# Kernel optimization log

Measured on AMD Instinct MI355X. Metric: run time of the kernel, lower is better.

## Reference

```python
import jax, jax.numpy as jnp
import numpy as np

B, T, U, D, INNER, VOCAB = 4, 256, 64, 512, 512, 2048

def setup_inputs() -> dict:
    key = jax.random.key(0)
    ks = jax.random.split(key, 6)
    return {
        "enc_state": jax.random.normal(ks[0], (B, T, D), jnp.float32),
        "dec_state": jax.random.normal(ks[1], (B, U, D), jnp.float32),
        "W1": jax.random.normal(ks[2], (2 * D, INNER), jnp.float32) * 0.02,
        "b1": jax.random.normal(ks[3], (INNER,), jnp.float32) * 0.02,
        "W2": jax.random.normal(ks[4], (INNER, VOCAB), jnp.float32) * 0.02,
        "b2": jax.random.normal(ks[5], (VOCAB,), jnp.float32) * 0.02,
    }

def reference(enc_state, dec_state, W1, b1, W2, b2):
    # concat([enc, dec]) @ W1 == enc @ W1[:D] + dec @ W1[D:]  (same math,
    # avoids materializing the [B,T,U,2D] repeat+cat tensor)
    d = enc_state.shape[-1]
    We, Wd = W1[:d], W1[d:]
    enc_proj = jnp.einsum('btd,dk->btk', enc_state, We)           # [B,T,INNER]
    dec_proj = jnp.einsum('bud,dk->buk', dec_state, Wd)           # [B,U,INNER]
    hidden = jnp.tanh(enc_proj[:, :, None, :] + dec_proj[:, None, :, :] + b1)  # [B,T,U,INNER]
    logits = jnp.einsum('btuk,kv->btuv', hidden, W2) + b2          # [B,T,U,VOCAB]
    return logits
```

## Files before the change

kernel.cpp:

```cpp
#include <hip/hip_runtime.h>
#include <hip/hip_bf16.h>

#define B_  4
#define T_  256
#define U_  64
#define D_  512
#define INNER_ 512
#define VOCAB_ 2048

typedef __attribute__((ext_vector_type(8))) short short8;
typedef __attribute__((ext_vector_type(4))) float f32x4;

__global__ __launch_bounds__(256) void proj_kernel(
    const float* __restrict__ enc, const float* __restrict__ dec,
    const float* __restrict__ W1, const float* __restrict__ b1,
    float* __restrict__ encP, float* __restrict__ decPb) {
  int ct = blockIdx.x;
  int rt = blockIdx.y;
  const float* src; float* dst; int kOff; int addB1; int rowBase;
  if (rt < 64) { src = enc; dst = encP; kOff = 0; addB1 = 0; rowBase = rt * 16; }
  else { src = dec; dst = decPb; kOff = D_; addB1 = 1; rowBase = (rt - 64) * 16; }

  __shared__ float As[16][D_];
  int tid = threadIdx.x;
  const float4* s4 = (const float4*)(src + (size_t)rowBase * D_);
  float4* a4 = (float4*)(&As[0][0]);
#pragma unroll
  for (int i = 0; i < 8; i++) a4[tid + 256 * i] = s4[tid + 256 * i];
  __syncthreads();

  int colQ = (tid & 31) * 4;
  int col = ct * 128 + colQ;
  int r0 = (tid >> 5) * 2;
  float a00=0,a01=0,a02=0,a03=0, a10=0,a11=0,a12=0,a13=0;
  const float* Wp = W1 + (size_t)kOff * INNER_ + col;
#pragma unroll 4
  for (int k = 0; k < D_; k++) {
    float4 w = *(const float4*)(Wp + (size_t)k * INNER_);
    float e0 = As[r0][k], e1 = As[r0 + 1][k];
    a00 += e0 * w.x; a01 += e0 * w.y; a02 += e0 * w.z; a03 += e0 * w.w;
    a10 += e1 * w.x; a11 += e1 * w.y; a12 += e1 * w.z; a13 += e1 * w.w;
  }
  float4 bb = {0,0,0,0};
  if (addB1) bb = *(const float4*)(b1 + col);
  float4 o0 = {a00 + bb.x, a01 + bb.y, a02 + bb.z, a03 + bb.w};
  float4 o1 = {a10 + bb.x, a11 + bb.y, a12 + bb.z, a13 + bb.w};
  *(float4*)(dst + (size_t)(rowBase + r0) * INNER_ + col) = o0;
  *(float4*)(dst + (size_t)(rowBase + r0 + 1) * INNER_ + col) = o1;
}

__global__ __launch_bounds__(256) void w2t_kernel(
    const float* __restrict__ W2, __hip_bfloat16* __restrict__ W2T) {
  __shared__ float tile[32][33];
  int vBase = blockIdx.x * 32;
  int kBase = blockIdx.y * 32;
  int tx = threadIdx.x & 31, ty = threadIdx.x >> 5;
#pragma unroll
  for (int i = 0; i < 32; i += 8)
    tile[ty + i][tx] = W2[(size_t)(kBase + ty + i) * VOCAB_ + vBase + tx];
  __syncthreads();
#pragma unroll
  for (int i = 0; i < 32; i += 8)
    W2T[(size_t)(vBase + ty + i) * INNER_ + kBase + tx] = __float2bfloat16(tile[tx][ty + i]);
}

__global__ __launch_bounds__(256) void hidden_kernel(
    const float* __restrict__ encP, const float* __restrict__ decPb,
    __hip_bfloat16* __restrict__ H) {
  int gid = blockIdx.x * 256 + threadIdx.x;
  int k0 = (gid & 63) * 8;
  int r = gid >> 6;
  int u = r & 63;
  int bt = r >> 6;
  int b = bt >> 8;
  const float4* e = (const float4*)(encP + (size_t)bt * 512 + k0);
  const float4* dv = (const float4*)(decPb + (size_t)(b * 64 + u) * 512 + k0);
  float4 e0 = e[0], e1 = e[1];
  float4 d0 = dv[0], d1 = dv[1];
  union { __hip_bfloat16 h[8]; uint4 v; } p;
  p.h[0] = __float2bfloat16(tanhf(e0.x + d0.x));
  p.h[1] = __float2bfloat16(tanhf(e0.y + d0.y));
  p.h[2] = __float2bfloat16(tanhf(e0.z + d0.z));
  p.h[3] = __float2bfloat16(tanhf(e0.w + d0.w));
  p.h[4] = __float2bfloat16(tanhf(e1.x + d1.x));
  p.h[5] = __float2bfloat16(tanhf(e1.y + d1.y));
  p.h[6] = __float2bfloat16(tanhf(e1.z + d1.z));
  p.h[7] = __float2bfloat16(tanhf(e1.w + d1.w));
  *(uint4*)((__hip_bfloat16*)H + (size_t)r * 512 + k0) = p.v;
}

__device__ inline void gload_lds16(const void* g, void* l) {
  __builtin_amdgcn_global_load_lds(
      (const __attribute__((address_space(1))) unsigned int*)g,
      (__attribute__((address_space(3))) unsigned int*)l, 16, 0, 0);
}

__global__ __launch_bounds__(256) void joint_gemm(
    const __hip_bfloat16* __restrict__ H, const __hip_bfloat16* __restrict__ W2T,
    const float* __restrict__ b2, float* __restrict__ out) {
  __shared__ __hip_bfloat16 As[128 * 64];
  __shared__ __hip_bfloat16 Bs[128 * 64];
  int ct = blockIdx.x;
  int rt = blockIdx.y;
  int tid = threadIdx.x;
  int wave = tid >> 6, lane = tid & 63;
  int wm = wave & 1, wn = wave >> 1;
  int rowBase = rt * 128, colBase = ct * 128;

  f32x4 acc[4][4];
#pragma unroll
  for (int ni = 0; ni < 4; ni++) {
    float bval = b2[colBase + wn * 64 + ni * 16 + (lane & 15)];
#pragma unroll
    for (int mi = 0; mi < 4; mi++) acc[mi][ni] = (f32x4){bval, bval, bval, bval};
  }

  int lrow = lane >> 3;
  int lk = (lane & 7) * 8;
  const __hip_bfloat16* Ag = H + (size_t)rowBase * 512;
  const __hip_bfloat16* Bg = W2T + (size_t)colBase * 512;

  for (int kt = 0; kt < 8; kt++) {
    int kOff = kt * 64;
    __syncthreads();
#pragma unroll
    for (int rnd = 0; rnd < 4; rnd++) {
      int rbase = wave * 8 + rnd * 32;
      gload_lds16(Ag + (size_t)(rbase + lrow) * 512 + kOff + lk, &As[rbase * 64]);
      gload_lds16(Bg + (size_t)(rbase + lrow) * 512 + kOff + lk, &Bs[rbase * 64]);
    }
    __syncthreads();
#pragma unroll
    for (int ks = 0; ks < 2; ks++) {
      short8 a[4], b[4];
      int kk = ks * 32 + (lane >> 4) * 8;
#pragma unroll
      for (int mi = 0; mi < 4; mi++)
        a[mi] = *(const short8*)&As[(wm * 64 + mi * 16 + (lane & 15)) * 64 + kk];
#pragma unroll
      for (int ni = 0; ni < 4; ni++)
        b[ni] = *(const short8*)&Bs[(wn * 64 + ni * 16 + (lane & 15)) * 64 + kk];
#pragma unroll
      for (int mi = 0; mi < 4; mi++)
#pragma unroll
        for (int ni = 0; ni < 4; ni++)
          acc[mi][ni] = __builtin_amdgcn_mfma_f32_16x16x32_bf16(a[mi], b[ni], acc[mi][ni], 0, 0, 0);
    }
  }

#pragma unroll
  for (int mi = 0; mi < 4; mi++) {
    int row = rowBase + wm * 64 + mi * 16 + ((lane >> 4) << 2);
#pragma unroll
    for (int ni = 0; ni < 4; ni++) {
      int col = colBase + wn * 64 + ni * 16 + (lane & 15);
#pragma unroll
      for (int j = 0; j < 4; j++)
        out[(size_t)(row + j) * VOCAB_ + col] = acc[mi][ni][j];
    }
  }
}

extern "C" void kernel_launch(void* const* d_in, const int* in_sizes, int n_in,
                              void* d_out, int out_size, void* d_ws, size_t ws_size,
                              hipStream_t stream) {
  const float* enc = (const float*)d_in[0];
  const float* dec = (const float*)d_in[1];
  const float* W1  = (const float*)d_in[2];
  const float* b1  = (const float*)d_in[3];
  const float* W2  = (const float*)d_in[4];
  const float* b2  = (const float*)d_in[5];
  float* out = (float*)d_out;

  char* ws = (char*)d_ws;
  float* encP  = (float*)ws;
  float* decPb = (float*)(ws + (2u << 20));
  __hip_bfloat16* W2T = (__hip_bfloat16*)(ws + (2u << 20) + (512u << 10));
  __hip_bfloat16* H   = (__hip_bfloat16*)(ws + (2u << 20) + (512u << 10) + (2u << 20));

  proj_kernel<<<dim3(4, 80), 256, 0, stream>>>(enc, dec, W1, b1, encP, decPb);
  w2t_kernel<<<dim3(64, 16), 256, 0, stream>>>(W2, W2T);
  hidden_kernel<<<16384, 256, 0, stream>>>(encP, decPb, H);
  joint_gemm<<<dim3(16, 512), 256, 0, stream>>>(H, W2T, b2, out);
}
```

Measured before the change: 784.9 us.

## Rewrite joint GEMM with 256x256 tiles, double-buffered swizzled LDS pipeline

```diff
diff --git a/kernel.cpp b/kernel.cpp
--- a/kernel.cpp
+++ b/kernel.cpp
@@ -95,68 +95,122 @@
       (__attribute__((address_space(3))) unsigned int*)l, 16, 0, 0);
 }
 
-__global__ __launch_bounds__(256) void joint_gemm(
+__global__ __launch_bounds__(512, 2) void joint_gemm(
     const __hip_bfloat16* __restrict__ H, const __hip_bfloat16* __restrict__ W2T,
     const float* __restrict__ b2, float* __restrict__ out) {
-  __shared__ __hip_bfloat16 As[128 * 64];
-  __shared__ __hip_bfloat16 Bs[128 * 64];
-  int ct = blockIdx.x;
-  int rt = blockIdx.y;
+  extern __shared__ char smem[];
   int tid = threadIdx.x;
-  int wave = tid >> 6, lane = tid & 63;
-  int wm = wave & 1, wn = wave >> 1;
-  int rowBase = rt * 128, colBase = ct * 128;
-
-  f32x4 acc[4][4];
-#pragma unroll
-  for (int ni = 0; ni < 4; ni++) {
-    float bval = b2[colBase + wn * 64 + ni * 16 + (lane & 15)];
-#pragma unroll
-    for (int mi = 0; mi < 4; mi++) acc[mi][ni] = (f32x4){bval, bval, bval, bval};
-  }
-
-  int lrow = lane >> 3;
-  int lk = (lane & 7) * 8;
-  const __hip_bfloat16* Ag = H + (size_t)rowBase * 512;
-  const __hip_bfloat16* Bg = W2T + (size_t)colBase * 512;
-
-  for (int kt = 0; kt < 8; kt++) {
-    int kOff = kt * 64;
-    __syncthreads();
-#pragma unroll
-    for (int rnd = 0; rnd < 4; rnd++) {
-      int rbase = wave * 8 + rnd * 32;
-      gload_lds16(Ag + (size_t)(rbase + lrow) * 512 + kOff + lk, &As[rbase * 64]);
-      gload_lds16(Bg + (size_t)(rbase + lrow) * 512 + kOff + lk, &Bs[rbase * 64]);
-    }
-    __syncthreads();
-#pragma unroll
-    for (int ks = 0; ks < 2; ks++) {
-      short8 a[4], b[4];
-      int kk = ks * 32 + (lane >> 4) * 8;
-#pragma unroll
-      for (int mi = 0; mi < 4; mi++)
-        a[mi] = *(const short8*)&As[(wm * 64 + mi * 16 + (lane & 15)) * 64 + kk];
-#pragma unroll
-      for (int ni = 0; ni < 4; ni++)
-        b[ni] = *(const short8*)&Bs[(wn * 64 + ni * 16 + (lane & 15)) * 64 + kk];
-#pragma unroll
-      for (int mi = 0; mi < 4; mi++)
-#pragma unroll
-        for (int ni = 0; ni < 4; ni++)
-          acc[mi][ni] = __builtin_amdgcn_mfma_f32_16x16x32_bf16(a[mi], b[ni], acc[mi][ni], 0, 0, 0);
-    }
-  }
-
-#pragma unroll
-  for (int mi = 0; mi < 4; mi++) {
-    int row = rowBase + wm * 64 + mi * 16 + ((lane >> 4) << 2);
+  int lane = tid & 63, wave = tid >> 6;
+  int wm = wave >> 2, wn = wave & 3;
+
+  int bid = blockIdx.x;
+  int wg = (bid & 7) * 256 + (bid >> 3);
+  int rt = wg >> 3;
+  int ct = wg & 7;
+  size_t rowBase = (size_t)rt * 256;
+  int colBase = ct * 256;
+
+  int srow = tid >> 3;
+  int kswz = ((tid & 7) ^ (srow & 7)) * 8;
+  const __hip_bfloat16* pA = H   + (rowBase + srow) * 512 + kswz;
+  const __hip_bfloat16* pB = W2T + (size_t)(colBase + srow) * 512 + kswz;
+  __hip_bfloat16* ldsA = (__hip_bfloat16*)smem;
+  __hip_bfloat16* ldsB = (__hip_bfloat16*)(smem + 65536);
+  int stageRow = wave * 8;
+
+#define STAGE(t, buf) do {                                                    \
+    const __hip_bfloat16* ga = pA + (size_t)(t) * 64;                         \
+    const __hip_bfloat16* gb = pB + (size_t)(t) * 64;                         \
+    __hip_bfloat16* la = ldsA + (buf) * 16384 + stageRow * 64;                \
+    __hip_bfloat16* lb = ldsB + (buf) * 16384 + stageRow * 64;                \
+    _Pragma("unroll")                                                         \
+    for (int j = 0; j < 4; j++) {                                             \
+      gload_lds16(ga + (size_t)j * 64 * 512, la + j * 64 * 64);               \
+      gload_lds16(gb + (size_t)j * 64 * 512, lb + j * 64 * 64);               \
+    } } while (0)
+
+  int lrA = wm * 128 + (lane & 15);
+  int lrB = wn * 64 + (lane & 15);
+  int sx = (lane & 7) * 16;
+  int q16 = (lane >> 4) * 16;
+  int offA0 = lrA * 128 + (q16 ^ sx);
+  int offA1 = lrA * 128 + ((64 + q16) ^ sx);
+  int offB0 = lrB * 128 + (q16 ^ sx);
+  int offB1 = lrB * 128 + ((64 + q16) ^ sx);
+
+  float bv[4];
+#pragma unroll
+  for (int ni = 0; ni < 4; ni++) bv[ni] = b2[colBase + wn * 64 + ni * 16 + (lane & 15)];
+  f32x4 acc[8][4];
+#pragma unroll
+  for (int mi = 0; mi < 8; mi++)
+#pragma unroll
+    for (int ni = 0; ni < 4; ni++)
+      acc[mi][ni] = (f32x4){bv[ni], bv[ni], bv[ni], bv[ni]};
+
+  asm volatile("s_waitcnt vmcnt(0)" ::: "memory");
+  __builtin_amdgcn_sched_barrier(0);
+
+  STAGE(0, 0);
+  STAGE(1, 1);
+
+#define KITER(t, buf, VMC, DOSTAGE) do {                                      \
+    asm volatile("s_waitcnt vmcnt(" #VMC ")" ::: "memory");                   \
+    __builtin_amdgcn_sched_barrier(0);                                        \
+    __builtin_amdgcn_s_barrier();                                             \
+    __builtin_amdgcn_sched_barrier(0);                                        \
+    const char* baA = (const char*)ldsA + (buf) * 32768;                      \
+    const char* baB = (const char*)ldsB + (buf) * 32768;                      \
+    short8 bfr[4][2], afr[4][2];                                              \
+    _Pragma("unroll") for (int ni = 0; ni < 4; ni++) {                        \
+      bfr[ni][0] = *(const short8*)(baB + offB0 + ni * 2048);                 \
+      bfr[ni][1] = *(const short8*)(baB + offB1 + ni * 2048); }               \
+    _Pragma("unroll") for (int mi = 0; mi < 4; mi++) {                        \
+      afr[mi][0] = *(const short8*)(baA + offA0 + mi * 2048);                 \
+      afr[mi][1] = *(const short8*)(baA + offA1 + mi * 2048); }               \
+    __builtin_amdgcn_s_setprio(1);                                            \
+    _Pragma("unroll") for (int mi = 0; mi < 4; mi++)                          \
+      _Pragma("unroll") for (int ni = 0; ni < 4; ni++) {                      \
+        acc[mi][ni] = __builtin_amdgcn_mfma_f32_16x16x32_bf16(                \
+            afr[mi][0], bfr[ni][0], acc[mi][ni], 0, 0, 0);                    \
+        acc[mi][ni] = __builtin_amdgcn_mfma_f32_16x16x32_bf16(                \
+            afr[mi][1], bfr[ni][1], acc[mi][ni], 0, 0, 0); }                  \
+    __builtin_amdgcn_s_setprio(0);                                            \
+    _Pragma("unroll") for (int mi = 0; mi < 4; mi++) {                        \
+      afr[mi][0] = *(const short8*)(baA + offA0 + 8192 + mi * 2048);          \
+      afr[mi][1] = *(const short8*)(baA + offA1 + 8192 + mi * 2048); }        \
+    asm volatile("s_waitcnt lgkmcnt(0)" ::: "memory");                        \
+    __builtin_amdgcn_sched_barrier(0);                                        \
+    __builtin_amdgcn_s_barrier();                                             \
+    __builtin_amdgcn_sched_barrier(0);                                        \
+    if (DOSTAGE) { STAGE((t) + 2, (buf)); }                                   \
+    __builtin_amdgcn_sched_barrier(0);                                        \
+    __builtin_amdgcn_s_setprio(1);                                            \
+    _Pragma("unroll") for (int mi = 0; mi < 4; mi++)                          \
+      _Pragma("unroll") for (int ni = 0; ni < 4; ni++) {                      \
+        acc[mi + 4][ni] = __builtin_amdgcn_mfma_f32_16x16x32_bf16(            \
+            afr[mi][0], bfr[ni][0], acc[mi + 4][ni], 0, 0, 0);                \
+        acc[mi + 4][ni] = __builtin_amdgcn_mfma_f32_16x16x32_bf16(            \
+            afr[mi][1], bfr[ni][1], acc[mi + 4][ni], 0, 0, 0); }              \
+    __builtin_amdgcn_s_setprio(0);                                            \
+  } while (0)
+
+#pragma unroll 2
+  for (int t = 0; t < 6; ++t) KITER(t, (t & 1), 8, 1);
+  KITER(6, 0, 8, 0);
+  KITER(7, 1, 0, 0);
+#undef KITER
+#undef STAGE
+
+#pragma unroll
+  for (int mi = 0; mi < 8; mi++) {
+    size_t row = rowBase + wm * 128 + mi * 16 + ((lane >> 4) << 2);
 #pragma unroll
     for (int ni = 0; ni < 4; ni++) {
       int col = colBase + wn * 64 + ni * 16 + (lane & 15);
 #pragma unroll
       for (int j = 0; j < 4; j++)
-        out[(size_t)(row + j) * VOCAB_ + col] = acc[mi][ni][j];
+        out[(row + j) * VOCAB_ + col] = acc[mi][ni][j];
     }
   }
 }
@@ -178,8 +232,15 @@
   __hip_bfloat16* W2T = (__hip_bfloat16*)(ws + (2u << 20) + (512u << 10));
   __hip_bfloat16* H   = (__hip_bfloat16*)(ws + (2u << 20) + (512u << 10) + (2u << 20));
 
+  static int smem_set = 0;
+  if (!smem_set) {
+    (void)hipFuncSetAttribute((const void*)joint_gemm,
+                              hipFuncAttributeMaxDynamicSharedMemorySize, 131072);
+    smem_set = 1;
+  }
+
   proj_kernel<<<dim3(4, 80), 256, 0, stream>>>(enc, dec, W1, b1, encP, decPb);
   w2t_kernel<<<dim3(64, 16), 256, 0, stream>>>(W2, W2T);
   hidden_kernel<<<16384, 256, 0, stream>>>(encP, decPb, H);
-  joint_gemm<<<dim3(16, 512), 256, 0, stream>>>(H, W2T, b2, out);
-}
+  joint_gemm<<<dim3(2048), 512, 131072, stream>>>(H, W2T, b2, out);
+}
```

Result: faster. 740.0 us (-5.7%).
